# Kernel tuning notes

Hardware: AMD Instinct MI355X
Metric: run time of the kernel (lower is better)

The kernel has to match this reference:

```python
import jax, jax.numpy as jnp
import numpy as np

B, N, L, K, C1 = 128, 300, 600, 19, 100  # batch, num_cnns, input_length, filter_size, fc hidden
PS = 7  # pool size == stride
LC = L - (K - 1)               # 582, conv output length
LP = (LC - PS) // PS + 1       # 83, pooled length
NC = 2                         # num_classes
EPS = 1e-5


def _bn(x, g, b, m, v):
    # eval-mode batchnorm, params broadcast along given axes already
    return g * (x - m) * jax.lax.rsqrt(v + EPS) + b


def setup_inputs() -> dict:
    key = jax.random.key(0)
    ks = jax.random.split(key, 20)
    f = lambda i, shape, s=0.1: (jax.random.normal(ks[i], shape, dtype=jnp.float32) * s)
    pv = lambda i, shape: (jax.random.uniform(ks[i], shape, dtype=jnp.float32) + 0.5)
    return {
        'x': jax.random.normal(ks[0], (B, 4, L), dtype=jnp.float32),
        'conv_w': f(1, (N, 4, K)), 'conv_b': f(2, (N,)),
        'bn1_g': pv(3, (N,)), 'bn1_b': f(4, (N,)), 'bn1_m': f(5, (N,)), 'bn1_v': pv(6, (N,)),
        'fc1_w': f(7, (N, C1, LP)), 'fc1_b': f(8, (N, C1)),
        'bn2_g': pv(9, (N, C1)), 'bn2_b': f(10, (N, C1)), 'bn2_m': f(11, (N, C1)), 'bn2_v': pv(12, (N, C1)),
        'fc2_w': f(13, (N, C1)), 'fc2_b': f(14, (N,)),
        'bn3_g': pv(15, (N,)), 'bn3_b': f(16, (N,)), 'bn3_m': f(17, (N,)), 'bn3_v': pv(18, (N,)),
        'final_w': f(19, (NC, N)), 'final_b': jnp.zeros((NC,), dtype=jnp.float32),
    }


def reference(x, conv_w, conv_b, bn1_g, bn1_b, bn1_m, bn1_v,
              fc1_w, fc1_b, bn2_g, bn2_b, bn2_m, bn2_v,
              fc2_w, fc2_b, bn3_g, bn3_b, bn3_m, bn3_v,
              final_w, final_b):
    # grouped conv on a repeated input == plain conv with 4 in-channels, N out-channels
    h = jax.lax.conv_general_dilated(x, conv_w, window_strides=(1,), padding='VALID',
                                     dimension_numbers=('NCH', 'OIH', 'NCH'))  # [B,N,582]
    h = h + conv_b[None, :, None]
    h = _bn(h, bn1_g[None, :, None], bn1_b[None, :, None], bn1_m[None, :, None], bn1_v[None, :, None])
    h = jnp.exp(h)
    # MaxPool1d(7,7): [B,N,582] -> [B,N,83]
    h = jax.lax.reduce_window(h, -jnp.inf, jax.lax.max,
                              window_dimensions=(1, 1, PS), window_strides=(1, 1, PS), padding='VALID')
    # grouped 1x1 conv == per-unit dense: [B,N,83] x [N,100,83] -> [B,N,100]
    h = jnp.einsum('bnp,nhp->bnh', h, fc1_w) + fc1_b[None]
    h = jax.nn.relu(_bn(h, bn2_g[None], bn2_b[None], bn2_m[None], bn2_v[None]))
    # second grouped 1x1 conv: [B,N,100] x [N,100] -> [B,N]
    h = jnp.einsum('bnh,nh->bn', h, fc2_w) + fc2_b[None]
    h = jax.nn.relu(_bn(h, bn3_g[None], bn3_b[None], bn3_m[None], bn3_v[None]))
    return h @ final_w.T + final_b  # [B,num_classes]
```

## Files before the change

kernel.cpp:

```cpp
#include <hip/hip_runtime.h>
#include <math.h>

#define EPS_ 1e-5f

__global__ __launch_bounds__(256) void kP(const float* __restrict__ fc1w,
                                          const float* __restrict__ conv_w,
                                          float* __restrict__ w1T,
                                          float* __restrict__ cw4) {
    const int blk = blockIdx.x, tid = threadIdx.x;
    if (blk < 300) {
        __shared__ float sm[83 * 101];
        for (int i = tid; i < 8300; i += 256) {
            const int h = i / 83, p = i - h * 83;
            sm[p * 101 + h] = fc1w[(size_t)blk * 8300 + i];
        }
        __syncthreads();
        for (int i = tid; i < 8300; i += 256) {
            const int p = i / 100, h = i - p * 100;
            w1T[(size_t)blk * 8300 + i] = sm[p * 101 + h];
        }
    } else {
        const int cq = blk - 300;
        const int c  = cq / 5;
        const int kq = cq - c * 5;
        for (int n = tid; n < 300; n += 256) {
            float4 v;
            const int k0 = 4 * kq;
            v.x = (k0 + 0 < 19) ? conv_w[n * 76 + c * 19 + k0 + 0] : 0.f;
            v.y = (k0 + 1 < 19) ? conv_w[n * 76 + c * 19 + k0 + 1] : 0.f;
            v.z = (k0 + 2 < 19) ? conv_w[n * 76 + c * 19 + k0 + 2] : 0.f;
            v.w = (k0 + 3 < 19) ? conv_w[n * 76 + c * 19 + k0 + 3] : 0.f;
            reinterpret_cast<float4*>(cw4)[(c * 5 + kq) * 300 + n] = v;
        }
    }
}

__global__ __launch_bounds__(64) void kA(
        const float* __restrict__ x,
        const float* __restrict__ cw4,
        const float* __restrict__ conv_b,
        const float* __restrict__ g1, const float* __restrict__ b1,
        const float* __restrict__ m1, const float* __restrict__ v1,
        float* __restrict__ pooled)
{
    const int id  = blockIdx.x;
    const int b   = id / 112;
    const int sub = id - b * 112;
    if (sub >= 105) return;
    const int ng  = sub / 21;
    const int pc  = sub - ng * 21;
    const int p0c = pc * 4;
    const int p0  = (p0c > 79) ? 79 : p0c;
    const int lane = threadIdx.x;
    const int n   = ng * 64 + lane;
    const int nc  = (n < 300) ? n : 299;

    const float4* w4 = reinterpret_cast<const float4*>(cw4);

    float acc[28];
    #pragma unroll
    for (int i = 0; i < 28; ++i) acc[i] = 0.f;

    #pragma unroll 1
    for (int c = 0; c < 4; ++c) {
        const float* xc = x + b * 2400 + c * 600 + 7 * p0;
        float xw[46];
        #pragma unroll
        for (int j = 0; j < 46; ++j) xw[j] = xc[j];
        #pragma unroll
        for (int kq = 0; kq < 5; ++kq) {
            const float4 wv = w4[(c * 5 + kq) * 300 + nc];
            const int ni = (kq == 4) ? 3 : 4;
            #pragma unroll
            for (int i = 0; i < ni; ++i) {
                const int k = 4 * kq + i;
                const float wvv = (i == 0) ? wv.x : (i == 1) ? wv.y
                                : (i == 2) ? wv.z : wv.w;
                #pragma unroll
                for (int p = 0; p < 4; ++p)
                    #pragma unroll
                    for (int q = 0; q < 7; ++q)
                        acc[p * 7 + q] = fmaf(xw[7 * p + q + k], wvv,
                                              acc[p * 7 + q]);
            }
        }
    }

    const float A1 = g1[nc] * rsqrtf(v1[nc] + EPS_);
    const float B1 = fmaf(A1, conv_b[nc] - m1[nc], b1[nc]);
    if (n < 300) {
        float* op = pooled + ((size_t)n * 83 + p0) * 128 + b;
        #pragma unroll
        for (int p = 0; p < 4; ++p) {
            float mx = -INFINITY;
            #pragma unroll
            for (int q = 0; q < 7; ++q)
                mx = fmaxf(mx, fmaf(A1, acc[p * 7 + q], B1));
            op[p * 128] = __expf(mx);
        }
    }
}

__global__ __launch_bounds__(256) void kB(
        const float* __restrict__ pooled,
        const float* __restrict__ w1T,
        const float* __restrict__ fc1b,
        const float* __restrict__ g2, const float* __restrict__ b2,
        const float* __restrict__ m2, const float* __restrict__ v2,
        const float* __restrict__ fc2w,
        const float* __restrict__ fc2b,
        const float* __restrict__ g3, const float* __restrict__ b3,
        const float* __restrict__ m3, const float* __restrict__ v3,
        float* __restrict__ sout)
{
    __shared__ float sRed[4][64];
    const int id = blockIdx.x;
    const int bh = id / 304;
    const int n  = id - bh * 304;
    const int tid  = threadIdx.x;
    const int lane = tid & 63;
    const int wv   = __builtin_amdgcn_readfirstlane(tid >> 6);
    const int h0   = wv * 28;
    const int nh   = (wv < 3) ? 28 : 16;
    const int bb   = bh * 64 + lane;

    float part = 0.f;
    if (n < 300) {
        const float* pp = pooled + (size_t)n * 83 * 128 + bb;
        const float* wp = w1T + (size_t)n * 8300 + h0;

        float acc[28];
        #pragma unroll
        for (int j = 0; j < 28; ++j) acc[j] = 0.f;

        if (nh == 28) {
            #pragma unroll 2
            for (int p = 0; p < 83; ++p) {
                const float pv = pp[p * 128];
                #pragma unroll
                for (int j = 0; j < 28; ++j)
                    acc[j] = fmaf(pv, wp[p * 100 + j], acc[j]);
            }
        } else {
            #pragma unroll 2
            for (int p = 0; p < 83; ++p) {
                const float pv = pp[p * 128];
                #pragma unroll
                for (int j = 0; j < 16; ++j)
                    acc[j] = fmaf(pv, wp[p * 100 + j], acc[j]);
            }
        }

        const int base = n * 100 + h0;
        for (int j = 0; j < nh; ++j) {
            const float A2 = g2[base + j] * rsqrtf(v2[base + j] + EPS_);
            const float C2 = fmaf(A2, fc1b[base + j] - m2[base + j], b2[base + j]);
            const float act = fmaxf(fmaf(A2, acc[j], C2), 0.f);
            part = fmaf(act, fc2w[base + j], part);
        }
    }
    sRed[wv][lane] = part;
    __syncthreads();
    if (tid < 64 && n < 300) {
        float s = sRed[0][tid] + sRed[1][tid] + sRed[2][tid] + sRed[3][tid];
        s += fc2b[n];
        const float A3 = g3[n] * rsqrtf(v3[n] + EPS_);
        const float z = fmaf(A3, s - m3[n], b3[n]);
        sout[n * 128 + bh * 64 + tid] = fmaxf(z, 0.f);
    }
}

__global__ __launch_bounds__(64) void kC(
        const float* __restrict__ sout,
        const float* __restrict__ fw,
        const float* __restrict__ fb,
        float* __restrict__ out)
{
    const int b = blockIdx.x, t = threadIdx.x;
    float a0 = 0.f, a1 = 0.f;
    for (int nn = t; nn < 300; nn += 64) {
        const float v = sout[nn * 128 + b];
        a0 = fmaf(v, fw[nn], a0);
        a1 = fmaf(v, fw[300 + nn], a1);
    }
    #pragma unroll
    for (int off = 32; off > 0; off >>= 1) {
        a0 += __shfl_xor(a0, off, 64);
        a1 += __shfl_xor(a1, off, 64);
    }
    if (t == 0) {
        out[b * 2 + 0] = a0 + fb[0];
        out[b * 2 + 1] = a1 + fb[1];
    }
}

extern "C" void kernel_launch(void* const* d_in, const int* in_sizes, int n_in,
                              void* d_out, int out_size, void* d_ws, size_t ws_size,
                              hipStream_t stream) {
    const float* x      = (const float*)d_in[0];
    const float* conv_w = (const float*)d_in[1];
    const float* conv_b = (const float*)d_in[2];
    const float* g1 = (const float*)d_in[3];
    const float* b1 = (const float*)d_in[4];
    const float* m1 = (const float*)d_in[5];
    const float* v1 = (const float*)d_in[6];
    const float* fc1_w = (const float*)d_in[7];
    const float* fc1_b = (const float*)d_in[8];
    const float* g2 = (const float*)d_in[9];
    const float* b2 = (const float*)d_in[10];
    const float* m2 = (const float*)d_in[11];
    const float* v2 = (const float*)d_in[12];
    const float* fc2_w = (const float*)d_in[13];
    const float* fc2_b = (const float*)d_in[14];
    const float* g3 = (const float*)d_in[15];
    const float* b3 = (const float*)d_in[16];
    const float* m3 = (const float*)d_in[17];
    const float* v3 = (const float*)d_in[18];
    const float* fw = (const float*)d_in[19];
    const float* fb = (const float*)d_in[20];
    float* out = (float*)d_out;

    float* pooled = (float*)d_ws;
    float* w1T    = pooled + (size_t)300 * 83 * 128;
    float* cw4    = w1T + (size_t)300 * 8300;
    float* sout   = cw4 + 24000;

    kP<<<320, 256, 0, stream>>>(fc1_w, conv_w, w1T, cw4);
    kA<<<128 * 112, 64, 0, stream>>>(x, cw4, conv_b, g1, b1, m1, v1, pooled);
    kB<<<608, 256, 0, stream>>>(pooled, w1T, fc1_b, g2, b2, m2, v2,
                                fc2_w, fc2_b, g3, b3, m3, v3, sout);
    kC<<<128, 64, 0, stream>>>(sout, fw, fb, out);
}
```

Baseline: 187.2 us.

## Drop fc1 weight transpose pass and read original layout directly in kB

Removes the per-call transpose of fc1_w into w1T from the prep kernel, so kP now only repacks conv weights. kB reads fc1_w in its native [N,100,83] layout, with each wave taking 25 hidden units and blocking the pooled dimension by 8, and the block index maps n and the batch half without padding blocks. This avoids writing and rereading roughly 10 MB of transposed weights. The trade is that weight reads inside kB become strided by 83 per hidden unit, which is uniform across a wave but may load less efficiently than the contiguous rows used before.

```diff
diff --git a/kernel.cpp b/kernel.cpp
--- a/kernel.cpp
+++ b/kernel.cpp
@@ -3,35 +3,19 @@
 
 #define EPS_ 1e-5f
 
-__global__ __launch_bounds__(256) void kP(const float* __restrict__ fc1w,
-                                          const float* __restrict__ conv_w,
-                                          float* __restrict__ w1T,
+__global__ __launch_bounds__(256) void kP(const float* __restrict__ conv_w,
                                           float* __restrict__ cw4) {
-    const int blk = blockIdx.x, tid = threadIdx.x;
-    if (blk < 300) {
-        __shared__ float sm[83 * 101];
-        for (int i = tid; i < 8300; i += 256) {
-            const int h = i / 83, p = i - h * 83;
-            sm[p * 101 + h] = fc1w[(size_t)blk * 8300 + i];
-        }
-        __syncthreads();
-        for (int i = tid; i < 8300; i += 256) {
-            const int p = i / 100, h = i - p * 100;
-            w1T[(size_t)blk * 8300 + i] = sm[p * 101 + h];
-        }
-    } else {
-        const int cq = blk - 300;
-        const int c  = cq / 5;
-        const int kq = cq - c * 5;
-        for (int n = tid; n < 300; n += 256) {
-            float4 v;
-            const int k0 = 4 * kq;
-            v.x = (k0 + 0 < 19) ? conv_w[n * 76 + c * 19 + k0 + 0] : 0.f;
-            v.y = (k0 + 1 < 19) ? conv_w[n * 76 + c * 19 + k0 + 1] : 0.f;
-            v.z = (k0 + 2 < 19) ? conv_w[n * 76 + c * 19 + k0 + 2] : 0.f;
-            v.w = (k0 + 3 < 19) ? conv_w[n * 76 + c * 19 + k0 + 3] : 0.f;
-            reinterpret_cast<float4*>(cw4)[(c * 5 + kq) * 300 + n] = v;
-        }
+    const int cq = blockIdx.x;
+    const int c  = cq / 5;
+    const int kq = cq - c * 5;
+    for (int n = threadIdx.x; n < 300; n += 256) {
+        float4 v;
+        const int k0 = 4 * kq;
+        v.x = (k0 + 0 < 19) ? conv_w[n * 76 + c * 19 + k0 + 0] : 0.f;
+        v.y = (k0 + 1 < 19) ? conv_w[n * 76 + c * 19 + k0 + 1] : 0.f;
+        v.z = (k0 + 2 < 19) ? conv_w[n * 76 + c * 19 + k0 + 2] : 0.f;
+        v.w = (k0 + 3 < 19) ? conv_w[n * 76 + c * 19 + k0 + 3] : 0.f;
+        reinterpret_cast<float4*>(cw4)[(c * 5 + kq) * 300 + n] = v;
     }
 }
 
@@ -103,7 +87,7 @@
 
 __global__ __launch_bounds__(256) void kB(
         const float* __restrict__ pooled,
-        const float* __restrict__ w1T,
+        const float* __restrict__ fc1w,
         const float* __restrict__ fc1b,
         const float* __restrict__ g2, const float* __restrict__ b2,
         const float* __restrict__ m2, const float* __restrict__ v2,
@@ -115,53 +99,58 @@
 {
     __shared__ float sRed[4][64];
     const int id = blockIdx.x;
-    const int bh = id / 304;
-    const int n  = id - bh * 304;
+    const int n  = id >> 1;
+    const int bh = id & 1;
     const int tid  = threadIdx.x;
     const int lane = tid & 63;
     const int wv   = __builtin_amdgcn_readfirstlane(tid >> 6);
-    const int h0   = wv * 28;
-    const int nh   = (wv < 3) ? 28 : 16;
+    const int h0   = wv * 25;
     const int bb   = bh * 64 + lane;
 
+    const float* pp = pooled + (size_t)n * 83 * 128 + bb;
+    const float* wb = fc1w + (size_t)n * 8300 + h0 * 83;
+
+    float acc[25];
+    #pragma unroll
+    for (int j = 0; j < 25; ++j) acc[j] = 0.f;
+
+    for (int pb = 0; pb < 10; ++pb) {
+        float pv[8];
+        #pragma unroll
+        for (int i = 0; i < 8; ++i) pv[i] = pp[(pb * 8 + i) * 128];
+        #pragma unroll
+        for (int j = 0; j < 25; ++j) {
+            const float* wr = wb + j * 83 + pb * 8;
+            #pragma unroll
+            for (int i = 0; i < 8; ++i)
+                acc[j] = fmaf(pv[i], wr[i], acc[j]);
+        }
+    }
+    {
+        float pv[3];
+        #pragma unroll
+        for (int i = 0; i < 3; ++i) pv[i] = pp[(80 + i) * 128];
+        #pragma unroll
+        for (int j = 0; j < 25; ++j) {
+            const float* wr = wb + j * 83 + 80;
+            #pragma unroll
+            for (int i = 0; i < 3; ++i)
+                acc[j] = fmaf(pv[i], wr[i], acc[j]);
+        }
+    }
+
+    const int base = n * 100 + h0;
     float part = 0.f;
-    if (n < 300) {
-        const float* pp = pooled + (size_t)n * 83 * 128 + bb;
-        const float* wp = w1T + (size_t)n * 8300 + h0;
-
-        float acc[28];
-        #pragma unroll
-        for (int j = 0; j < 28; ++j) acc[j] = 0.f;
-
-        if (nh == 28) {
-            #pragma unroll 2
-            for (int p = 0; p < 83; ++p) {
-                const float pv = pp[p * 128];
-                #pragma unroll
-                for (int j = 0; j < 28; ++j)
-                    acc[j] = fmaf(pv, wp[p * 100 + j], acc[j]);
-            }
-        } else {
-            #pragma unroll 2
-            for (int p = 0; p < 83; ++p) {
-                const float pv = pp[p * 128];
-                #pragma unroll
-                for (int j = 0; j < 16; ++j)
-                    acc[j] = fmaf(pv, wp[p * 100 + j], acc[j]);
-            }
-        }
-
-        const int base = n * 100 + h0;
-        for (int j = 0; j < nh; ++j) {
-            const float A2 = g2[base + j] * rsqrtf(v2[base + j] + EPS_);
-            const float C2 = fmaf(A2, fc1b[base + j] - m2[base + j], b2[base + j]);
-            const float act = fmaxf(fmaf(A2, acc[j], C2), 0.f);
-            part = fmaf(act, fc2w[base + j], part);
-        }
+    #pragma unroll
+    for (int j = 0; j < 25; ++j) {
+        const float A2 = g2[base + j] * rsqrtf(v2[base + j] + EPS_);
+        const float C2 = fmaf(A2, fc1b[base + j] - m2[base + j], b2[base + j]);
+        const float act = fmaxf(fmaf(A2, acc[j], C2), 0.f);
+        part = fmaf(act, fc2w[base + j], part);
     }
     sRed[wv][lane] = part;
     __syncthreads();
-    if (tid < 64 && n < 300) {
+    if (tid < 64) {
         float s = sRed[0][tid] + sRed[1][tid] + sRed[2][tid] + sRed[3][tid];
         s += fc2b[n];
         const float A3 = g3[n] * rsqrtf(v3[n] + EPS_);
@@ -221,13 +210,12 @@
     float* out = (float*)d_out;
 
     float* pooled = (float*)d_ws;
-    float* w1T    = pooled + (size_t)300 * 83 * 128;
-    float* cw4    = w1T + (size_t)300 * 8300;
+    float* cw4    = pooled + (size_t)300 * 83 * 128;
     float* sout   = cw4 + 24000;
 
-    kP<<<320, 256, 0, stream>>>(fc1_w, conv_w, w1T, cw4);
+    kP<<<20, 256, 0, stream>>>(conv_w, cw4);
     kA<<<128 * 112, 64, 0, stream>>>(x, cw4, conv_b, g1, b1, m1, v1, pooled);
-    kB<<<608, 256, 0, stream>>>(pooled, w1T, fc1_b, g2, b2, m2, v2,
+    kB<<<600, 256, 0, stream>>>(pooled, fc1_w, fc1_b, g2, b2, m2, v2,
                                 fc2_w, fc2_b, g3, b3, m3, v3, sout);
     kC<<<128, 64, 0, stream>>>(sout, fw, fb, out);
 }
```

Result: slower. 195.2 us (+4.3%).

## Stage padded fc1 weights in LDS and compute two batch columns per thread in kB

Applied to the files above, without the earlier changes.

kP now writes the transposed fc1 weights padded to 112 columns per row. kB copies each unit's weights into shared memory with float4 loads and runs one block per unit covering all 128 batch items, two per lane. The inner loop reads weights as LDS float4 and pooled values as float2. Each block reuses the staged weights across twice as many FMAs, but the grid halves to 300 blocks, which may underfill the GPU, and the larger accumulator array raises register pressure.

```diff
diff --git a/kernel.cpp b/kernel.cpp
--- a/kernel.cpp
+++ b/kernel.cpp
@@ -5,7 +5,7 @@
 
 __global__ __launch_bounds__(256) void kP(const float* __restrict__ fc1w,
                                           const float* __restrict__ conv_w,
-                                          float* __restrict__ w1T,
+                                          float* __restrict__ w1Tp,
                                           float* __restrict__ cw4) {
     const int blk = blockIdx.x, tid = threadIdx.x;
     if (blk < 300) {
@@ -15,9 +15,9 @@
             sm[p * 101 + h] = fc1w[(size_t)blk * 8300 + i];
         }
         __syncthreads();
-        for (int i = tid; i < 8300; i += 256) {
-            const int p = i / 100, h = i - p * 100;
-            w1T[(size_t)blk * 8300 + i] = sm[p * 101 + h];
+        for (int i = tid; i < 9296; i += 256) {
+            const int p = i / 112, h = i - p * 112;
+            w1Tp[(size_t)blk * 9296 + i] = (h < 100) ? sm[p * 101 + h] : 0.f;
         }
     } else {
         const int cq = blk - 300;
@@ -101,9 +101,9 @@
     }
 }
 
-__global__ __launch_bounds__(256) void kB(
+__global__ __launch_bounds__(256, 2) void kB(
         const float* __restrict__ pooled,
-        const float* __restrict__ w1T,
+        const float* __restrict__ w1Tp,
         const float* __restrict__ fc1b,
         const float* __restrict__ g2, const float* __restrict__ b2,
         const float* __restrict__ m2, const float* __restrict__ v2,
@@ -113,60 +113,69 @@
         const float* __restrict__ m3, const float* __restrict__ v3,
         float* __restrict__ sout)
 {
-    __shared__ float sRed[4][64];
-    const int id = blockIdx.x;
-    const int bh = id / 304;
-    const int n  = id - bh * 304;
-    const int tid  = threadIdx.x;
+    __shared__ __align__(16) float sW[83 * 112];
+    __shared__ float2 sRed[4][64];
+    const int n   = blockIdx.x;
+    const int tid = threadIdx.x;
+
+    {
+        const float4* src = reinterpret_cast<const float4*>(w1Tp + (size_t)n * 9296);
+        float4* dst = reinterpret_cast<float4*>(sW);
+        for (int i = tid; i < 2324; i += 256) dst[i] = src[i];
+    }
+    __syncthreads();
+
     const int lane = tid & 63;
     const int wv   = __builtin_amdgcn_readfirstlane(tid >> 6);
     const int h0   = wv * 28;
-    const int nh   = (wv < 3) ? 28 : 16;
-    const int bb   = bh * 64 + lane;
-
-    float part = 0.f;
-    if (n < 300) {
-        const float* pp = pooled + (size_t)n * 83 * 128 + bb;
-        const float* wp = w1T + (size_t)n * 8300 + h0;
-
-        float acc[28];
-        #pragma unroll
-        for (int j = 0; j < 28; ++j) acc[j] = 0.f;
-
-        if (nh == 28) {
-            #pragma unroll 2
-            for (int p = 0; p < 83; ++p) {
-                const float pv = pp[p * 128];
-                #pragma unroll
-                for (int j = 0; j < 28; ++j)
-                    acc[j] = fmaf(pv, wp[p * 100 + j], acc[j]);
-            }
-        } else {
-            #pragma unroll 2
-            for (int p = 0; p < 83; ++p) {
-                const float pv = pp[p * 128];
-                #pragma unroll
-                for (int j = 0; j < 16; ++j)
-                    acc[j] = fmaf(pv, wp[p * 100 + j], acc[j]);
-            }
-        }
-
-        const int base = n * 100 + h0;
-        for (int j = 0; j < nh; ++j) {
-            const float A2 = g2[base + j] * rsqrtf(v2[base + j] + EPS_);
-            const float C2 = fmaf(A2, fc1b[base + j] - m2[base + j], b2[base + j]);
-            const float act = fmaxf(fmaf(A2, acc[j], C2), 0.f);
-            part = fmaf(act, fc2w[base + j], part);
-        }
-    }
-    sRed[wv][lane] = part;
+    const int b0   = lane * 2;
+
+    const float* pp = pooled + (size_t)n * 83 * 128 + b0;
+
+    float acc[28][2];
+    #pragma unroll
+    for (int j = 0; j < 28; ++j) { acc[j][0] = 0.f; acc[j][1] = 0.f; }
+
+    #pragma unroll 4
+    for (int p = 0; p < 83; ++p) {
+        const float2 pv = *reinterpret_cast<const float2*>(pp + p * 128);
+        const float* wrow = sW + p * 112 + h0;
+        #pragma unroll
+        for (int jq = 0; jq < 7; ++jq) {
+            const float4 w = *reinterpret_cast<const float4*>(wrow + 4 * jq);
+            acc[jq * 4 + 0][0] = fmaf(w.x, pv.x, acc[jq * 4 + 0][0]);
+            acc[jq * 4 + 0][1] = fmaf(w.x, pv.y, acc[jq * 4 + 0][1]);
+            acc[jq * 4 + 1][0] = fmaf(w.y, pv.x, acc[jq * 4 + 1][0]);
+            acc[jq * 4 + 1][1] = fmaf(w.y, pv.y, acc[jq * 4 + 1][1]);
+            acc[jq * 4 + 2][0] = fmaf(w.z, pv.x, acc[jq * 4 + 2][0]);
+            acc[jq * 4 + 2][1] = fmaf(w.z, pv.y, acc[jq * 4 + 2][1]);
+            acc[jq * 4 + 3][0] = fmaf(w.w, pv.x, acc[jq * 4 + 3][0]);
+            acc[jq * 4 + 3][1] = fmaf(w.w, pv.y, acc[jq * 4 + 3][1]);
+        }
+    }
+
+    const int nh = (wv < 3) ? 28 : 16;
+    float p0s = 0.f, p1s = 0.f;
+    for (int j = 0; j < nh; ++j) {
+        const int hi = n * 100 + h0 + j;
+        const float A2 = g2[hi] * rsqrtf(v2[hi] + EPS_);
+        const float C2 = fmaf(A2, fc1b[hi] - m2[hi], b2[hi]);
+        const float w2 = fc2w[hi];
+        p0s = fmaf(fmaxf(fmaf(A2, acc[j][0], C2), 0.f), w2, p0s);
+        p1s = fmaf(fmaxf(fmaf(A2, acc[j][1], C2), 0.f), w2, p1s);
+    }
+    sRed[wv][lane] = make_float2(p0s, p1s);
     __syncthreads();
-    if (tid < 64 && n < 300) {
-        float s = sRed[0][tid] + sRed[1][tid] + sRed[2][tid] + sRed[3][tid];
+
+    if (tid < 128) {
+        const int l = tid >> 1, r = tid & 1;
+        float s = (r == 0)
+            ? (sRed[0][l].x + sRed[1][l].x + sRed[2][l].x + sRed[3][l].x)
+            : (sRed[0][l].y + sRed[1][l].y + sRed[2][l].y + sRed[3][l].y);
         s += fc2b[n];
         const float A3 = g3[n] * rsqrtf(v3[n] + EPS_);
         const float z = fmaf(A3, s - m3[n], b3[n]);
-        sout[n * 128 + bh * 64 + tid] = fmaxf(z, 0.f);
+        sout[n * 128 + tid] = fmaxf(z, 0.f);
     }
 }
 
@@ -221,13 +230,13 @@
     float* out = (float*)d_out;
 
     float* pooled = (float*)d_ws;
-    float* w1T    = pooled + (size_t)300 * 83 * 128;
-    float* cw4    = w1T + (size_t)300 * 8300;
+    float* w1Tp   = pooled + (size_t)300 * 83 * 128;
+    float* cw4    = w1Tp + (size_t)300 * 9296;
     float* sout   = cw4 + 24000;
 
-    kP<<<320, 256, 0, stream>>>(fc1_w, conv_w, w1T, cw4);
+    kP<<<320, 256, 0, stream>>>(fc1_w, conv_w, w1Tp, cw4);
     kA<<<128 * 112, 64, 0, stream>>>(x, cw4, conv_b, g1, b1, m1, v1, pooled);
-    kB<<<608, 256, 0, stream>>>(pooled, w1T, fc1_b, g2, b2, m2, v2,
+    kB<<<300, 256, 0, stream>>>(pooled, w1Tp, fc1_b, g2, b2, m2, v2,
                                 fc2_w, fc2_b, g3, b3, m3, v3, sout);
     kC<<<128, 64, 0, stream>>>(sout, fw, fb, out);
 }
```

After: 186.7 us. No clear change (-0.3%).
